# Kernel optimization log

Hardware: AMD Instinct MI355X
Metric: run time of the kernel (lower is better)

The kernel has to match this reference:

```python
import jax, jax.numpy as jnp
import numpy as np
from jax import lax

N = 8192

def _conv(x, w, b):
    # x: NCHW, w: OIHW, valid conv stride 1
    y = lax.conv_general_dilated(x, w, (1, 1), 'VALID',
                                 dimension_numbers=('NCHW', 'OIHW', 'NCHW'))
    return y + b[None, :, None, None]

def _maxpool2(x):
    return lax.reduce_window(x, -jnp.inf, lax.max, (1, 1, 2, 2), (1, 1, 2, 2), 'VALID')

def setup_inputs() -> dict:
    key = jax.random.key(0)
    ks = jax.random.split(key, 13)
    def rn(k, shape, scale):
        return jax.random.normal(k, shape, dtype=jnp.float32) * scale
    inp = {}
    inp['x'] = jax.random.normal(ks[0], (N, 3, 32, 32), dtype=jnp.float32)
    inp['W1'] = rn(ks[1], (6, 3, 5, 5), 0.1)
    inp['b1'] = rn(ks[2], (6,), 0.1)
    inp['W2'] = rn(ks[3], (16, 6, 5, 5), 0.08)
    inp['b2'] = rn(ks[4], (16,), 0.1)
    inp['Wf1'] = rn(ks[5], (120, 400), 0.05)
    inp['bf1'] = rn(ks[6], (120,), 0.05)
    inp['Wf2'] = rn(ks[7], (84, 120), 0.09)
    inp['bf2'] = rn(ks[8], (84,), 0.09)
    inp['Wg'] = rn(ks[9], (10, 84), 0.1)    # GATConv fc weight (no bias)
    inp['attn_l'] = rn(ks[10], (10,), 0.3)  # a_l (src)
    inp['attn_r'] = rn(ks[11], (10,), 0.3)  # a_r (dst)
    inp['bg'] = rn(ks[12], (10,), 0.1)      # GATConv output bias
    return inp

def reference(x, W1, b1, W2, b2, Wf1, bf1, Wf2, bf2, Wg, attn_l, attn_r, bg):
    # CNN feature extractor (LeNet style)
    h = _maxpool2(jax.nn.relu(_conv(x, W1, b1)))   # [N,6,14,14]
    h = _maxpool2(jax.nn.relu(_conv(h, W2, b2)))   # [N,16,5,5]
    h = h.reshape(-1, 16 * 5 * 5)                  # [N,400]
    h = jax.nn.relu(h @ Wf1.T + bf1)               # [N,120]
    h = jax.nn.relu(h @ Wf2.T + bf2)               # [N,84]
    # Single-head GAT over fully-connected graph (incl. self-loops):
    # equivalent dense formulation of DGL GATConv(84,10,1)
    z = h @ Wg.T                                    # [N,10]
    el = z @ attn_l                                 # src scores [N]
    er = z @ attn_r                                 # dst scores [N]
    # e[i,j]: edge src=j -> dst=i
    e = jax.nn.leaky_relu(er[:, None] + el[None, :], negative_slope=0.2)  # [N,N]
    alpha = jax.nn.softmax(e, axis=1)               # softmax over incoming edges
    out = alpha @ z + bg                            # [N,10]
    return out
```

## Files before the change

### kernel.cpp

```cpp
#include <hip/hip_runtime.h>
#include <hip/hip_bf16.h>

typedef _Float16 half8 __attribute__((ext_vector_type(8)));
typedef __attribute__((aligned(8))) half8 half8_a8;
typedef float floatx4 __attribute__((ext_vector_type(4)));

#define LOG2E 1.44269504088896340736f

__device__ __forceinline__ float pool4_dpp(float v) {
  int s1 = __builtin_amdgcn_update_dpp(0, __float_as_int(v), 0xB1, 0xF, 0xF, true);
  float v1 = fmaxf(v, __int_as_float(s1));
  int s2 = __builtin_amdgcn_update_dpp(0, __float_as_int(v1), 0x4E, 0xF, 0xF, true);
  return fmaxf(v1, __int_as_float(s2));
}

__device__ __forceinline__ unsigned f2mono(float f) {
  unsigned u = __float_as_uint(f);
  return (u & 0x80000000u) ? ~u : (u | 0x80000000u);
}
__device__ __forceinline__ float mono2f(unsigned u) {
  return (u & 0x80000000u) ? __uint_as_float(u & 0x7fffffffu)
                           : __uint_as_float(~u);
}

__global__ __launch_bounds__(256) void k_prep(const float* __restrict__ Wf1,
    const float* __restrict__ Wf2, const float* __restrict__ Wg,
    const float* __restrict__ W1, const float* __restrict__ W2,
    _Float16* __restrict__ w1f, _Float16* __restrict__ w2f,
    _Float16* __restrict__ wgf, _Float16* __restrict__ B1,
    _Float16* __restrict__ B2M, unsigned* __restrict__ emx) {
  const int i = blockIdx.x * 256 + threadIdx.x;
  if (i == 0) emx[0] = 0u;
  if (i < 53248) {
    const int n = i / 416, k = i - n * 416;
    w1f[i] = (_Float16)((n < 120 && k < 400) ? Wf1[n * 400 + k] : 0.f);
  } else if (i < 65536) {
    const int j = i - 53248;
    const int n = j >> 7, k = j & 127;
    w2f[j] = (_Float16)((n < 84 && k < 120) ? Wf2[n * 120 + k] : 0.f);
  } else if (i < 67072) {
    const int g = i - 65536;
    const int n = g / 96, k = g - n * 96;
    wgf[g] = (_Float16)((n < 10 && k < 84) ? Wg[n * 84 + k] : 0.f);
  } else if (i < 73216) {
    const int g = i - 67072;
    const int n = g / 192, k = g - n * 192;
    const int co = n >> 2, cy = (n >> 1) & 1, cx = n & 1;
    const int pidx = k >> 3, j = k & 7;
    const int r = pidx >> 2, ci = pidx & 3;
    float v = 0.f;
    if (co < 6 && ci < 3) {
      const int ky = r - cy, kx = j - cx;
      if (ky >= 0 && ky < 5 && kx >= 0 && kx < 5)
        v = W1[((co * 3 + ci) * 5 + ky) * 5 + kx];
    }
    B1[g] = (_Float16)v;
  } else if (i < 77312) {
    const int g = i - 73216;
    const int n = g >> 8, k = g & 255;
    float v = 0.f;
    if (k < 240) {
      const int ci = k / 40, rem = k - ci * 40, r = rem >> 3, j = rem & 7;
      if (j < 5) v = W2[((n * 6 + ci) * 5 + r) * 5 + j];
    }
    B2M[g] = (_Float16)v;
  }
}

__global__ __launch_bounds__(512) void k_convs(const float* __restrict__ x,
    const _Float16* __restrict__ B1, const float* __restrict__ b1,
    const _Float16* __restrict__ B2M, const float* __restrict__ b2,
    _Float16* __restrict__ h2) {
  __shared__ __align__(16) char sm[71616];
  _Float16* h1L = (_Float16*)(sm + 62208);
  const int t = threadIdx.x;
  const int n0 = blockIdx.x * 4;
  const int w8 = t >> 6, lane = t & 63;
  const int l16 = lane & 15, q = lane >> 4;

  const float4* x4 = (const float4*)(x + (size_t)n0 * 3072);
  for (int i = t; i < 3072; i += 512) {
    const float4 v = x4[i];
    const int img = i / 768;
    const int ii = i - img * 768;
    const int ci = ii >> 8, rem2 = ii & 255;
    const int y = rem2 >> 3, c = rem2 & 7;
    union { _Float16 h[2]; unsigned u; } p01, p23;
    p01.h[0] = (_Float16)v.x; p01.h[1] = (_Float16)v.y;
    p23.h[0] = (_Float16)v.z; p23.h[1] = (_Float16)v.w;
    char* row = sm + img * 15552 + ci * 5184 + y * 80;
    *(uint2*)(row + 8 * c) = make_uint2(p01.u, p23.u);
    *(unsigned*)(row + 2596 + 8 * c) = p01.u;
    *(unsigned*)(row + 2600 + 8 * c) = p23.u;
  }
  if (t < 384) {
    const int img = t / 96, tt = t - img * 96;
    const int ci = tt >> 5, y = tt & 31;
    *(unsigned*)(sm + img * 15552 + ci * 5184 + 2596 + y * 80 + 64) = 0u;
  }
  if (t < 64) {
    const int im = t >> 4;
    h2[(size_t)(n0 + im) * 416 + 400 + (t & 15)] = (_Float16)0.f;
  }
  __syncthreads();

  {
    const int img = w8 >> 1, wl = w8 & 1;
    const int px = l16;
    const int colOff = (px & 1) ? (2596 + 4 * px) : (4 * px);
    const char* base = sm + img * 15552 + ((q == 3) ? 0 : q * 5184) + colOff;
    half8 bfr[2][6];
#pragma unroll
    for (int nt = 0; nt < 2; nt++)
#pragma unroll
      for (int kc = 0; kc < 6; kc++)
        bfr[nt][kc] =
            *(const half8*)(B1 + (size_t)(nt * 16 + l16) * 192 + kc * 32 + q * 8);
    const int co_n = l16 >> 2;
    const int co1 = 4 + co_n;
    const float bias0 = b1[co_n];
    const float bias1 = (co1 < 6) ? b1[co1] : 0.f;
    const int py0 = wl * 7;
    const int py1 = py0 + 7;
    half8 a[6];
#pragma unroll
    for (int r = 0; r < 6; r++)
      a[r] = *(const half8_a8*)(base + (2 * py0 + r) * 80);
    _Float16* dstb = h1L + img * 1176;
    const bool store_lane = (l16 & 3) == 0;
    for (int py = py0; py < py1; ++py) {
      floatx4 acc0, acc1;
#pragma unroll
      for (int r = 0; r < 4; r++) { acc0[r] = 0.f; acc1[r] = 0.f; }
#pragma unroll
      for (int kc = 0; kc < 6; kc++) {
        acc0 = __builtin_amdgcn_mfma_f32_16x16x32_f16(a[kc], bfr[0][kc], acc0, 0, 0, 0);
        acc1 = __builtin_amdgcn_mfma_f32_16x16x32_f16(a[kc], bfr[1][kc], acc1, 0, 0, 0);
      }
      if (py < py1 - 1) {
        a[0] = a[2]; a[1] = a[3]; a[2] = a[4]; a[3] = a[5];
        a[4] = *(const half8_a8*)(base + (2 * py + 6) * 80);
        a[5] = *(const half8_a8*)(base + (2 * py + 7) * 80);
      }
      float p0[4], p1[4];
#pragma unroll
      for (int r = 0; r < 4; r++) {
        p0[r] = fmaxf(pool4_dpp(acc0[r]) + bias0, 0.f);
        p1[r] = fmaxf(pool4_dpp(acc1[r]) + bias1, 0.f);
      }
      if (store_lane) {
        union { _Float16 h[2]; unsigned u; } s01, s23;
        s01.h[0] = (_Float16)p0[0]; s01.h[1] = (_Float16)p0[1];
        s23.h[0] = (_Float16)p0[2]; s23.h[1] = (_Float16)p0[3];
        _Float16* dst = dstb + co_n * 196 + py * 14 + q * 4;
        *(unsigned*)dst = s01.u;
        if (q < 3) *(unsigned*)(dst + 2) = s23.u;
        if (co1 < 6) {
          union { _Float16 h[2]; unsigned u; } t01, t23;
          t01.h[0] = (_Float16)p1[0]; t01.h[1] = (_Float16)p1[1];
          t23.h[0] = (_Float16)p1[2]; t23.h[1] = (_Float16)p1[3];
          _Float16* dst1 = dstb + co1 * 196 + py * 14 + q * 4;
          *(unsigned*)dst1 = t01.u;
          if (q < 3) *(unsigned*)(dst1 + 2) = t23.u;
        }
      }
    }
  }
  __syncthreads();

  if (t < 336) {
    const int img = t / 84, rem = t - img * 84;
    const int ci = rem / 14, y = rem - ci * 14;
    const unsigned* src = (const unsigned*)(h1L + img * 1176 + ci * 196 + y * 14);
    unsigned u[10];
#pragma unroll
    for (int k = 0; k < 7; k++) u[k] = src[k];
    u[7] = 0u; u[8] = 0u; u[9] = 0u;
    char* base = sm + img * 11184 + ci * 1864 + y * 32;
#pragma unroll
    for (int ww = 0; ww < 8; ww++) {
      *(unsigned*)(base + 4 * ww) = u[ww];
      *(unsigned*)(base + 464 + 4 * ww) = (u[ww] >> 16) | (u[ww + 1] << 16);
      *(unsigned*)(base + 928 + 4 * ww) = u[ww + 1];
      *(unsigned*)(base + 1392 + 4 * ww) = (u[ww + 1] >> 16) | (u[ww + 2] << 16);
    }
  }
  __syncthreads();

  {
    int C2[8];
#pragma unroll
    for (int kc = 0; kc < 8; kc++) {
      const int pidx = kc * 4 + q;
      C2[kc] = (pidx < 30) ? (pidx / 5) * 1864 + (pidx % 5) * 32 : 0;
    }
    half8 bfr[8];
#pragma unroll
    for (int kc = 0; kc < 8; kc++)
      bfr[kc] = *(const half8*)(B2M + (size_t)l16 * 256 + kc * 32 + q * 8);
    const float bias = b2[l16];
    for (int mt = w8; mt < 26; mt += 8) {
      const int m = min(mt * 16 + l16, 399);
      const int pos = m >> 2, cy = (m >> 1) & 1, cx = m & 1;
      const int img = pos / 25, p = pos - img * 25;
      const int py = p / 5, px = p - py * 5;
      const int h = 2 * px + cx, s = h & 3;
      const char* base =
          sm + img * 11184 + s * 464 + (2 * py + cy) * 32 + (h - s) * 2;
      half8 a[8];
#pragma unroll
      for (int kc = 0; kc < 8; kc++) a[kc] = *(const half8_a8*)(base + C2[kc]);
      floatx4 acc;
#pragma unroll
      for (int r = 0; r < 4; r++) acc[r] = 0.f;
#pragma unroll
      for (int kc = 0; kc < 8; kc++)
        acc = __builtin_amdgcn_mfma_f32_16x16x32_f16(a[kc], bfr[kc], acc, 0, 0, 0);
      const float v = fmaxf(fmaxf(acc[0], acc[1]), fmaxf(acc[2], acc[3]));
      const int posL = mt * 4 + q;
      if (posL < 100) {
        const int im = posL / 25, pp = posL - im * 25;
        h2[(size_t)(n0 + im) * 416 + l16 * 25 + pp] =
            (_Float16)fmaxf(v + bias, 0.f);
      }
    }
  }
}

__global__ __launch_bounds__(256) void k_mlp(
    const _Float16* __restrict__ h2, const _Float16* __restrict__ w1,
    const float* __restrict__ bf1, const _Float16* __restrict__ w2,
    const float* __restrict__ bf2, const _Float16* __restrict__ wg,
    const float* __restrict__ al, const float* __restrict__ ar,
    _Float16* __restrict__ zT, float* __restrict__ el, float* __restrict__ er,
    unsigned* __restrict__ emx) {
  __shared__ __align__(16) _Float16 h3s[32 * 136];
  __shared__ __align__(16) _Float16 h4s[32 * 104];
  __shared__ float zs[32 * 17];
  const int t = threadIdx.x;
  const int w = t >> 6, lane = t & 63;
  const int l16 = lane & 15, q = lane >> 4;
  const int row0 = blockIdx.x * 32;
  for (int i = t; i < 2176; i += 256) ((float*)h3s)[i] = 0.f;
  for (int i = t; i < 1664; i += 256) ((float*)h4s)[i] = 0.f;
  const int rt = w & 1, cg = w >> 1;
  const int am = row0 + rt * 16 + l16;
  floatx4 acc[4];
#pragma unroll
  for (int ct = 0; ct < 4; ct++)
#pragma unroll
    for (int r = 0; r < 4; r++) acc[ct][r] = 0.f;
  const half8* Ag = (const half8*)(h2 + (size_t)am * 416 + q * 8);
  for (int kc = 0; kc < 13; kc++) {
    half8 a = Ag[kc * 4];
#pragma unroll
    for (int ct = 0; ct < 4; ct++) {
      const int n = cg * 64 + ct * 16 + l16;
      half8 b = *(const half8*)(w1 + (size_t)n * 416 + kc * 32 + q * 8);
      acc[ct] = __builtin_amdgcn_mfma_f32_16x16x32_f16(a, b, acc[ct], 0, 0, 0);
    }
  }
  __syncthreads();
#pragma unroll
  for (int ct = 0; ct < 4; ct++) {
    const int n = cg * 64 + ct * 16 + l16;
    if (n < 120) {
      const float bias = bf1[n];
#pragma unroll
      for (int r = 0; r < 4; r++) {
        const int rr = rt * 16 + q * 4 + r;
        h3s[rr * 136 + n] = (_Float16)fmaxf(acc[ct][r] + bias, 0.f);
      }
    }
  }
  __syncthreads();
  const int cbase2 = (w >> 1) * 3;
  floatx4 acc2[3];
#pragma unroll
  for (int ct = 0; ct < 3; ct++)
#pragma unroll
    for (int r = 0; r < 4; r++) acc2[ct][r] = 0.f;
  const _Float16* A2 = h3s + (rt * 16 + l16) * 136 + q * 8;
  for (int kc = 0; kc < 4; kc++) {
    half8 a = *(const half8*)(A2 + kc * 32);
#pragma unroll
    for (int ct = 0; ct < 3; ct++) {
      const int n = (cbase2 + ct) * 16 + l16;
      half8 b = *(const half8*)(w2 + (size_t)n * 128 + kc * 32 + q * 8);
      acc2[ct] = __builtin_amdgcn_mfma_f32_16x16x32_f16(a, b, acc2[ct], 0, 0, 0);
    }
  }
  __syncthreads();
#pragma unroll
  for (int ct = 0; ct < 3; ct++) {
    const int n = (cbase2 + ct) * 16 + l16;
    if (n < 84) {
      const float bias = bf2[n];
#pragma unroll
      for (int r = 0; r < 4; r++) {
        const int rr = rt * 16 + q * 4 + r;
        h4s[rr * 104 + n] = (_Float16)fmaxf(acc2[ct][r] + bias, 0.f);
      }
    }
  }
  __syncthreads();
  if (w < 2) {
    floatx4 acc3;
#pragma unroll
    for (int r = 0; r < 4; r++) acc3[r] = 0.f;
    const _Float16* A3 = h4s + (w * 16 + l16) * 104 + q * 8;
    for (int kc = 0; kc < 3; kc++) {
      half8 a = *(const half8*)(A3 + kc * 32);
      half8 b = *(const half8*)(wg + (size_t)l16 * 96 + kc * 32 + q * 8);
      acc3 = __builtin_amdgcn_mfma_f32_16x16x32_f16(a, b, acc3, 0, 0, 0);
    }
#pragma unroll
    for (int r = 0; r < 4; r++) {
      const int rr = w * 16 + q * 4 + r;
      zs[rr * 17 + l16] = acc3[r];
    }
  }
  __syncthreads();
  if (t < 32) {
    float e1 = 0.f, e2 = 0.f;
#pragma unroll
    for (int d = 0; d < 10; d++) {
      const float zv = zs[t * 17 + d];
      e1 += zv * al[d];
      e2 += zv * ar[d];
    }
    const float elv = e1 * LOG2E;
    el[row0 + t] = elv;
    er[row0 + t] = e2 * LOG2E;
    float m = elv;
#pragma unroll
    for (int off = 16; off > 0; off >>= 1)
      m = fmaxf(m, __shfl_down(m, off, 32));
    if (t == 0) atomicMax(emx, f2mono(m));
  }
  for (int idx = t; idx < 352; idx += 256) {
    const int d = idx >> 5, c = idx & 31;
    zT[(size_t)d * 8192 + row0 + c] =
        (d < 10) ? (_Float16)zs[c * 17 + d] : (_Float16)1.0f;
  }
}

__global__ __launch_bounds__(1024) void k_attn(const _Float16* __restrict__ zT,
    const float* __restrict__ el, const float* __restrict__ er,
    const unsigned* __restrict__ emx, const float* __restrict__ bg,
    float* __restrict__ out) {
  __shared__ float red[8][2][16][12];
  const int t = threadIdx.x;
  const int w = t >> 6, lane = t & 63;
  const int l16 = lane & 15, q = lane >> 4;
  const int isub = w & 1, js = w >> 1;
  const int row0 = blockIdx.x * 32;
  const int itile = row0 + isub * 16;
  const int jb = js * 1024;
  const float mx = mono2f(emx[0]);
  const float eri = er[itile + l16];
  const float s0 = eri + mx;
  const float mi = fmaxf(s0, 0.2f * s0);
  floatx4 acc;
#pragma unroll
  for (int r = 0; r < 4; r++) acc[r] = 0.f;
  const float* elp = el + jb + q * 8;
  const _Float16* ztp = zT + (size_t)l16 * 8192 + jb + q * 8;
  for (int jc = 0; jc < 32; jc++) {
    const float4 e0 = *(const float4*)(elp + jc * 32);
    const float4 e1 = *(const float4*)(elp + jc * 32 + 4);
    float wf[8];
    const float ej[8] = {e0.x, e0.y, e0.z, e0.w, e1.x, e1.y, e1.z, e1.w};
#pragma unroll
    for (int u = 0; u < 8; u++) {
      const float s = eri + ej[u];
      const float lr = fmaxf(s, 0.2f * s);
      wf[u] = exp2f(lr - mi);
    }
    half8 a;
#pragma unroll
    for (int u = 0; u < 8; u++) a[u] = (_Float16)wf[u];
    const half8 b = *(const half8*)(ztp + jc * 32);
    acc = __builtin_amdgcn_mfma_f32_16x16x32_f16(a, b, acc, 0, 0, 0);
  }
  if (l16 < 11) {
#pragma unroll
    for (int r = 0; r < 4; r++) red[js][isub][q * 4 + r][l16] = acc[r];
  }
  __syncthreads();
  if (t < 320) {
    const int ii = t / 10, d = t - (t / 10) * 10;
    const int i1 = ii >> 4, i2 = ii & 15;
    float num = 0.f, den = 0.f;
#pragma unroll
    for (int s = 0; s < 8; s++) {
      num += red[s][i1][i2][d];
      den += red[s][i1][i2][10];
    }
    out[(size_t)(row0 + ii) * 10 + d] = num / den + bg[d];
  }
}

extern "C" void kernel_launch(void* const* d_in, const int* in_sizes, int n_in,
                              void* d_out, int out_size, void* d_ws, size_t ws_size,
                              hipStream_t stream) {
  const float* x   = (const float*)d_in[0];
  const float* W1  = (const float*)d_in[1];
  const float* b1  = (const float*)d_in[2];
  const float* W2  = (const float*)d_in[3];
  const float* b2  = (const float*)d_in[4];
  const float* Wf1 = (const float*)d_in[5];
  const float* bf1 = (const float*)d_in[6];
  const float* Wf2 = (const float*)d_in[7];
  const float* bf2 = (const float*)d_in[8];
  const float* Wg  = (const float*)d_in[9];
  const float* al  = (const float*)d_in[10];
  const float* ar  = (const float*)d_in[11];
  const float* bg  = (const float*)d_in[12];
  float* out = (float*)d_out;

  float* ws = (float*)d_ws;
  float* p = ws + (size_t)8192 * 588;
  _Float16* h2f = (_Float16*)p;
  p += (size_t)8192 * 208;
  _Float16* zTf = (_Float16*)p; p += 65536;
  float* el  = p; p += 8192;
  float* er  = p; p += 8192;
  unsigned* emx = (unsigned*)p; p += 16;
  _Float16* w1f = (_Float16*)p; p += 26624;
  _Float16* w2f = (_Float16*)p; p += 6144;
  _Float16* wgf = (_Float16*)p; p += 768;
  _Float16* B1g = (_Float16*)p; p += 3072;
  _Float16* B2g = (_Float16*)p; p += 2048;

  k_prep<<<302, 256, 0, stream>>>(Wf1, Wf2, Wg, W1, W2, w1f, w2f, wgf, B1g, B2g, emx);
  k_convs<<<2048, 512, 0, stream>>>(x, B1g, b1, B2g, b2, h2f);
  k_mlp<<<256, 256, 0, stream>>>(h2f, w1f, bf1, w2f, bf2, wgf, al, ar, zTf, el, er, emx);
  k_attn<<<256, 1024, 0, stream>>>(zTf, el, er, emx, bg, out);
}
```

Baseline: 256.6 us.

## Process one image per conv block with smaller LDS footprint and padded strides

The fused conv kernel now handles one image per 256-thread block instead of four images per 512-thread block, which shrinks shared memory from about 72KB to about 18KB. The aim is to fit more blocks per CU and raise occupancy. The LDS strides for the input planes and the shifted conv2 staging buffers are also re-padded (5200, 560/2240, 40-byte rows), probably to cut bank conflicts. In exchange, work splits unevenly across the 4 waves: 14 conv1 rows become 3/4/3/4, and 7 conv2 M-tiles cover only 25 positions, leaving some lanes idle. Per-block setup cost is also amortized over fewer images.

Measured after the change: 274.0 us. 1.07x slower.

```diff
diff --git a/kernel.cpp b/kernel.cpp
--- a/kernel.cpp
+++ b/kernel.cpp
@@ -67,48 +67,43 @@
   }
 }
 
-__global__ __launch_bounds__(512) void k_convs(const float* __restrict__ x,
+__global__ __launch_bounds__(256) void k_convs(const float* __restrict__ x,
     const _Float16* __restrict__ B1, const float* __restrict__ b1,
     const _Float16* __restrict__ B2M, const float* __restrict__ b2,
     _Float16* __restrict__ h2) {
-  __shared__ __align__(16) char sm[71616];
-  _Float16* h1L = (_Float16*)(sm + 62208);
+  __shared__ __align__(16) char sm[17952];
+  _Float16* h1L = (_Float16*)(sm + 15600);
   const int t = threadIdx.x;
-  const int n0 = blockIdx.x * 4;
-  const int w8 = t >> 6, lane = t & 63;
+  const int n0 = blockIdx.x;
+  const int w4 = t >> 6, lane = t & 63;
   const int l16 = lane & 15, q = lane >> 4;
 
   const float4* x4 = (const float4*)(x + (size_t)n0 * 3072);
-  for (int i = t; i < 3072; i += 512) {
+  for (int i = t; i < 768; i += 256) {
     const float4 v = x4[i];
-    const int img = i / 768;
-    const int ii = i - img * 768;
-    const int ci = ii >> 8, rem2 = ii & 255;
+    const int ci = i >> 8, rem2 = i & 255;
     const int y = rem2 >> 3, c = rem2 & 7;
     union { _Float16 h[2]; unsigned u; } p01, p23;
     p01.h[0] = (_Float16)v.x; p01.h[1] = (_Float16)v.y;
     p23.h[0] = (_Float16)v.z; p23.h[1] = (_Float16)v.w;
-    char* row = sm + img * 15552 + ci * 5184 + y * 80;
+    char* row = sm + ci * 5200 + y * 80;
     *(uint2*)(row + 8 * c) = make_uint2(p01.u, p23.u);
     *(unsigned*)(row + 2596 + 8 * c) = p01.u;
     *(unsigned*)(row + 2600 + 8 * c) = p23.u;
   }
-  if (t < 384) {
-    const int img = t / 96, tt = t - img * 96;
-    const int ci = tt >> 5, y = tt & 31;
-    *(unsigned*)(sm + img * 15552 + ci * 5184 + 2596 + y * 80 + 64) = 0u;
-  }
-  if (t < 64) {
-    const int im = t >> 4;
-    h2[(size_t)(n0 + im) * 416 + 400 + (t & 15)] = (_Float16)0.f;
+  if (t < 96) {
+    const int ci = t >> 5, y = t & 31;
+    *(unsigned*)(sm + ci * 5200 + 2596 + y * 80 + 64) = 0u;
+  }
+  if (t < 16) {
+    h2[(size_t)n0 * 416 + 400 + t] = (_Float16)0.f;
   }
   __syncthreads();
 
   {
-    const int img = w8 >> 1, wl = w8 & 1;
     const int px = l16;
     const int colOff = (px & 1) ? (2596 + 4 * px) : (4 * px);
-    const char* base = sm + img * 15552 + ((q == 3) ? 0 : q * 5184) + colOff;
+    const char* base = sm + ((q == 3) ? 0 : q * 5200) + colOff;
     half8 bfr[2][6];
 #pragma unroll
     for (int nt = 0; nt < 2; nt++)
@@ -120,13 +115,12 @@
     const int co1 = 4 + co_n;
     const float bias0 = b1[co_n];
     const float bias1 = (co1 < 6) ? b1[co1] : 0.f;
-    const int py0 = wl * 7;
-    const int py1 = py0 + 7;
+    const int py0 = (7 * w4) >> 1;
+    const int py1 = (7 * (w4 + 1)) >> 1;
     half8 a[6];
 #pragma unroll
     for (int r = 0; r < 6; r++)
       a[r] = *(const half8_a8*)(base + (2 * py0 + r) * 80);
-    _Float16* dstb = h1L + img * 1176;
     const bool store_lane = (l16 & 3) == 0;
     for (int py = py0; py < py1; ++py) {
       floatx4 acc0, acc1;
@@ -152,14 +146,14 @@
         union { _Float16 h[2]; unsigned u; } s01, s23;
         s01.h[0] = (_Float16)p0[0]; s01.h[1] = (_Float16)p0[1];
         s23.h[0] = (_Float16)p0[2]; s23.h[1] = (_Float16)p0[3];
-        _Float16* dst = dstb + co_n * 196 + py * 14 + q * 4;
+        _Float16* dst = h1L + co_n * 196 + py * 14 + q * 4;
         *(unsigned*)dst = s01.u;
         if (q < 3) *(unsigned*)(dst + 2) = s23.u;
         if (co1 < 6) {
           union { _Float16 h[2]; unsigned u; } t01, t23;
           t01.h[0] = (_Float16)p1[0]; t01.h[1] = (_Float16)p1[1];
           t23.h[0] = (_Float16)p1[2]; t23.h[1] = (_Float16)p1[3];
-          _Float16* dst1 = dstb + co1 * 196 + py * 14 + q * 4;
+          _Float16* dst1 = h1L + co1 * 196 + py * 14 + q * 4;
           *(unsigned*)dst1 = t01.u;
           if (q < 3) *(unsigned*)(dst1 + 2) = t23.u;
         }
@@ -168,21 +162,23 @@
   }
   __syncthreads();
 
-  if (t < 336) {
-    const int img = t / 84, rem = t - img * 84;
-    const int ci = rem / 14, y = rem - ci * 14;
-    const unsigned* src = (const unsigned*)(h1L + img * 1176 + ci * 196 + y * 14);
-    unsigned u[10];
-#pragma unroll
-    for (int k = 0; k < 7; k++) u[k] = src[k];
-    u[7] = 0u; u[8] = 0u; u[9] = 0u;
-    char* base = sm + img * 11184 + ci * 1864 + y * 32;
-#pragma unroll
-    for (int ww = 0; ww < 8; ww++) {
+  if (t < 168) {
+    const int ci = t / 28, rem = t - ci * 28;
+    const int y = rem >> 1, g = rem & 1;
+    const unsigned* src = (const unsigned*)(h1L + ci * 196 + y * 14);
+    unsigned u[6];
+#pragma unroll
+    for (int k = 0; k < 6; k++) {
+      const int idx = 4 * g + k;
+      u[k] = (idx < 7) ? src[idx] : 0u;
+    }
+    char* base = sm + ci * 2240 + y * 40 + 16 * g;
+#pragma unroll
+    for (int ww = 0; ww < 4; ww++) {
       *(unsigned*)(base + 4 * ww) = u[ww];
-      *(unsigned*)(base + 464 + 4 * ww) = (u[ww] >> 16) | (u[ww + 1] << 16);
-      *(unsigned*)(base + 928 + 4 * ww) = u[ww + 1];
-      *(unsigned*)(base + 1392 + 4 * ww) = (u[ww + 1] >> 16) | (u[ww + 2] << 16);
+      *(unsigned*)(base + 560 + 4 * ww) = (u[ww] >> 16) | (u[ww + 1] << 16);
+      *(unsigned*)(base + 1120 + 4 * ww) = u[ww + 1];
+      *(unsigned*)(base + 1680 + 4 * ww) = (u[ww + 1] >> 16) | (u[ww + 2] << 16);
     }
   }
   __syncthreads();
@@ -192,21 +188,19 @@
 #pragma unroll
     for (int kc = 0; kc < 8; kc++) {
       const int pidx = kc * 4 + q;
-      C2[kc] = (pidx < 30) ? (pidx / 5) * 1864 + (pidx % 5) * 32 : 0;
+      C2[kc] = (pidx < 30) ? (pidx / 5) * 2240 + (pidx % 5) * 40 : 0;
     }
     half8 bfr[8];
 #pragma unroll
     for (int kc = 0; kc < 8; kc++)
       bfr[kc] = *(const half8*)(B2M + (size_t)l16 * 256 + kc * 32 + q * 8);
     const float bias = b2[l16];
-    for (int mt = w8; mt < 26; mt += 8) {
-      const int m = min(mt * 16 + l16, 399);
+    for (int mt = w4; mt < 7; mt += 4) {
+      const int m = min(mt * 16 + l16, 99);
       const int pos = m >> 2, cy = (m >> 1) & 1, cx = m & 1;
-      const int img = pos / 25, p = pos - img * 25;
-      const int py = p / 5, px = p - py * 5;
+      const int py = pos / 5, px = pos - py * 5;
       const int h = 2 * px + cx, s = h & 3;
-      const char* base =
-          sm + img * 11184 + s * 464 + (2 * py + cy) * 32 + (h - s) * 2;
+      const char* base = sm + s * 560 + (2 * py + cy) * 40 + (h - s) * 2;
       half8 a[8];
 #pragma unroll
       for (int kc = 0; kc < 8; kc++) a[kc] = *(const half8_a8*)(base + C2[kc]);
@@ -218,9 +212,8 @@
         acc = __builtin_amdgcn_mfma_f32_16x16x32_f16(a[kc], bfr[kc], acc, 0, 0, 0);
       const float v = fmaxf(fmaxf(acc[0], acc[1]), fmaxf(acc[2], acc[3]));
       const int posL = mt * 4 + q;
-      if (posL < 100) {
-        const int im = posL / 25, pp = posL - im * 25;
-        h2[(size_t)(n0 + im) * 416 + l16 * 25 + pp] =
+      if (posL < 25) {
+        h2[(size_t)n0 * 416 + l16 * 25 + posL] =
             (_Float16)fmaxf(v + bias, 0.f);
       }
     }
@@ -434,7 +427,7 @@
   _Float16* B2g = (_Float16*)p; p += 2048;
 
   k_prep<<<302, 256, 0, stream>>>(Wf1, Wf2, Wg, W1, W2, w1f, w2f, wgf, B1g, B2g, emx);
-  k_convs<<<2048, 512, 0, stream>>>(x, B1g, b1, B2g, b2, h2f);
+  k_convs<<<8192, 256, 0, stream>>>(x, B1g, b1, B2g, b2, h2f);
   k_mlp<<<256, 256, 0, stream>>>(h2f, w1f, bf1, w2f, bf2, wgf, al, ar, zTf, el, er, emx);
   k_attn<<<256, 1024, 0, stream>>>(zTf, el, er, emx, bg, out);
 }
```

## Shrink conv blocks to three images and 256 threads for higher occupancy

Applied to the files above, without the earlier changes.

The fused conv kernel now processes three images per block with 256 threads, cutting LDS from about 70KB to about 53KB so three blocks can share a CU (launch_bounds 256,3). Work is redistributed: conv1 rows are assigned per wave across images with full reloads of the six A rows instead of a sliding window, the re-layout step is split into half-row tasks, and weight fragments are hoisted to kernel start. Bounds checks handle the partial last block. This trades some redundant LDS reads and register pressure for better latency hiding from more resident waves.

Result: no change. 261.7 us (+2.0%).

```diff
diff --git a/kernel.cpp b/kernel.cpp
--- a/kernel.cpp
+++ b/kernel.cpp
@@ -67,21 +67,39 @@
   }
 }
 
-__global__ __launch_bounds__(512) void k_convs(const float* __restrict__ x,
+__global__ __launch_bounds__(256, 3) void k_convs(const float* __restrict__ x,
     const _Float16* __restrict__ B1, const float* __restrict__ b1,
     const _Float16* __restrict__ B2M, const float* __restrict__ b2,
     _Float16* __restrict__ h2) {
-  __shared__ __align__(16) char sm[71616];
-  _Float16* h1L = (_Float16*)(sm + 62208);
+  __shared__ __align__(16) char sm[53712];
+  _Float16* h1L = (_Float16*)(sm + 46656);
   const int t = threadIdx.x;
-  const int n0 = blockIdx.x * 4;
-  const int w8 = t >> 6, lane = t & 63;
+  const int n0 = blockIdx.x * 3;
+  const int w4 = t >> 6, lane = t & 63;
   const int l16 = lane & 15, q = lane >> 4;
 
+  half8 bfr1[2][6];
+#pragma unroll
+  for (int nt = 0; nt < 2; nt++)
+#pragma unroll
+    for (int kc = 0; kc < 6; kc++)
+      bfr1[nt][kc] =
+          *(const half8*)(B1 + (size_t)(nt * 16 + l16) * 192 + kc * 32 + q * 8);
+  half8 bfr2[8];
+#pragma unroll
+  for (int kc = 0; kc < 8; kc++)
+    bfr2[kc] = *(const half8*)(B2M + (size_t)l16 * 256 + kc * 32 + q * 8);
+  const int co_n = l16 >> 2;
+  const int co1 = 4 + co_n;
+  const float bias1_0 = b1[co_n];
+  const float bias1_1 = (co1 < 6) ? b1[co1] : 0.f;
+  const float bias2 = b2[l16];
+
   const float4* x4 = (const float4*)(x + (size_t)n0 * 3072);
-  for (int i = t; i < 3072; i += 512) {
-    const float4 v = x4[i];
+  for (int i = t; i < 2304; i += 256) {
     const int img = i / 768;
+    float4 v = make_float4(0.f, 0.f, 0.f, 0.f);
+    if (n0 + img < 8192) v = x4[i];
     const int ii = i - img * 768;
     const int ci = ii >> 8, rem2 = ii & 255;
     const int y = rem2 >> 3, c = rem2 & 7;
@@ -93,73 +111,60 @@
     *(unsigned*)(row + 2596 + 8 * c) = p01.u;
     *(unsigned*)(row + 2600 + 8 * c) = p23.u;
   }
-  if (t < 384) {
+  if (t < 192) {
     const int img = t / 96, tt = t - img * 96;
     const int ci = tt >> 5, y = tt & 31;
     *(unsigned*)(sm + img * 15552 + ci * 5184 + 2596 + y * 80 + 64) = 0u;
-  }
-  if (t < 64) {
+    if (t < 96) {
+      const int ci2 = t >> 5, y2 = t & 31;
+      *(unsigned*)(sm + 2 * 15552 + ci2 * 5184 + 2596 + y2 * 80 + 64) = 0u;
+    }
+  }
+  if (t < 48) {
     const int im = t >> 4;
-    h2[(size_t)(n0 + im) * 416 + 400 + (t & 15)] = (_Float16)0.f;
+    if (n0 + im < 8192)
+      h2[(size_t)(n0 + im) * 416 + 400 + (t & 15)] = (_Float16)0.f;
   }
   __syncthreads();
 
   {
-    const int img = w8 >> 1, wl = w8 & 1;
     const int px = l16;
     const int colOff = (px & 1) ? (2596 + 4 * px) : (4 * px);
-    const char* base = sm + img * 15552 + ((q == 3) ? 0 : q * 5184) + colOff;
-    half8 bfr[2][6];
-#pragma unroll
-    for (int nt = 0; nt < 2; nt++)
-#pragma unroll
-      for (int kc = 0; kc < 6; kc++)
-        bfr[nt][kc] =
-            *(const half8*)(B1 + (size_t)(nt * 16 + l16) * 192 + kc * 32 + q * 8);
-    const int co_n = l16 >> 2;
-    const int co1 = 4 + co_n;
-    const float bias0 = b1[co_n];
-    const float bias1 = (co1 < 6) ? b1[co1] : 0.f;
-    const int py0 = wl * 7;
-    const int py1 = py0 + 7;
-    half8 a[6];
-#pragma unroll
-    for (int r = 0; r < 6; r++)
-      a[r] = *(const half8_a8*)(base + (2 * py0 + r) * 80);
-    _Float16* dstb = h1L + img * 1176;
+    const char* cbase = sm + ((q == 3) ? 0 : q * 5184) + colOff;
     const bool store_lane = (l16 & 3) == 0;
-    for (int py = py0; py < py1; ++py) {
+    for (int u = w4; u < 42; u += 4) {
+      const int img = u / 14, py = u - img * 14;
+      const char* base = cbase + img * 15552;
+      half8 a[6];
+#pragma unroll
+      for (int r = 0; r < 6; r++)
+        a[r] = *(const half8_a8*)(base + (2 * py + r) * 80);
       floatx4 acc0, acc1;
 #pragma unroll
       for (int r = 0; r < 4; r++) { acc0[r] = 0.f; acc1[r] = 0.f; }
 #pragma unroll
       for (int kc = 0; kc < 6; kc++) {
-        acc0 = __builtin_amdgcn_mfma_f32_16x16x32_f16(a[kc], bfr[0][kc], acc0, 0, 0, 0);
-        acc1 = __builtin_amdgcn_mfma_f32_16x16x32_f16(a[kc], bfr[1][kc], acc1, 0, 0, 0);
-      }
-      if (py < py1 - 1) {
-        a[0] = a[2]; a[1] = a[3]; a[2] = a[4]; a[3] = a[5];
-        a[4] = *(const half8_a8*)(base + (2 * py + 6) * 80);
-        a[5] = *(const half8_a8*)(base + (2 * py + 7) * 80);
+        acc0 = __builtin_amdgcn_mfma_f32_16x16x32_f16(a[kc], bfr1[0][kc], acc0, 0, 0, 0);
+        acc1 = __builtin_amdgcn_mfma_f32_16x16x32_f16(a[kc], bfr1[1][kc], acc1, 0, 0, 0);
       }
       float p0[4], p1[4];
 #pragma unroll
       for (int r = 0; r < 4; r++) {
-        p0[r] = fmaxf(pool4_dpp(acc0[r]) + bias0, 0.f);
-        p1[r] = fmaxf(pool4_dpp(acc1[r]) + bias1, 0.f);
+        p0[r] = fmaxf(pool4_dpp(acc0[r]) + bias1_0, 0.f);
+        p1[r] = fmaxf(pool4_dpp(acc1[r]) + bias1_1, 0.f);
       }
       if (store_lane) {
         union { _Float16 h[2]; unsigned u; } s01, s23;
         s01.h[0] = (_Float16)p0[0]; s01.h[1] = (_Float16)p0[1];
         s23.h[0] = (_Float16)p0[2]; s23.h[1] = (_Float16)p0[3];
-        _Float16* dst = dstb + co_n * 196 + py * 14 + q * 4;
+        _Float16* dst = h1L + img * 1176 + co_n * 196 + py * 14 + q * 4;
         *(unsigned*)dst = s01.u;
         if (q < 3) *(unsigned*)(dst + 2) = s23.u;
         if (co1 < 6) {
           union { _Float16 h[2]; unsigned u; } t01, t23;
           t01.h[0] = (_Float16)p1[0]; t01.h[1] = (_Float16)p1[1];
           t23.h[0] = (_Float16)p1[2]; t23.h[1] = (_Float16)p1[3];
-          _Float16* dst1 = dstb + co1 * 196 + py * 14 + q * 4;
+          _Float16* dst1 = h1L + img * 1176 + co1 * 196 + py * 14 + q * 4;
           *(unsigned*)dst1 = t01.u;
           if (q < 3) *(unsigned*)(dst1 + 2) = t23.u;
         }
@@ -168,21 +173,24 @@
   }
   __syncthreads();
 
-  if (t < 336) {
-    const int img = t / 84, rem = t - img * 84;
-    const int ci = rem / 14, y = rem - ci * 14;
+  for (int uu = t; uu < 504; uu += 256) {
+    const int img = uu / 168, rem = uu - img * 168;
+    const int ci = rem / 28, r2 = rem - ci * 28;
+    const int y = r2 >> 1, g = r2 & 1;
     const unsigned* src = (const unsigned*)(h1L + img * 1176 + ci * 196 + y * 14);
-    unsigned u[10];
-#pragma unroll
-    for (int k = 0; k < 7; k++) u[k] = src[k];
-    u[7] = 0u; u[8] = 0u; u[9] = 0u;
-    char* base = sm + img * 11184 + ci * 1864 + y * 32;
-#pragma unroll
-    for (int ww = 0; ww < 8; ww++) {
-      *(unsigned*)(base + 4 * ww) = u[ww];
-      *(unsigned*)(base + 464 + 4 * ww) = (u[ww] >> 16) | (u[ww + 1] << 16);
-      *(unsigned*)(base + 928 + 4 * ww) = u[ww + 1];
-      *(unsigned*)(base + 1392 + 4 * ww) = (u[ww + 1] >> 16) | (u[ww + 2] << 16);
+    unsigned u6[6];
+#pragma unroll
+    for (int k = 0; k < 6; k++) {
+      const int idx = 4 * g + k;
+      u6[k] = (idx < 7) ? src[idx] : 0u;
+    }
+    char* base = sm + img * 11136 + ci * 1856 + y * 32 + 16 * g;
+#pragma unroll
+    for (int ww = 0; ww < 4; ww++) {
+      *(unsigned*)(base + 4 * ww) = u6[ww];
+      *(unsigned*)(base + 464 + 4 * ww) = (u6[ww] >> 16) | (u6[ww + 1] << 16);
+      *(unsigned*)(base + 928 + 4 * ww) = u6[ww + 1];
+      *(unsigned*)(base + 1392 + 4 * ww) = (u6[ww + 1] >> 16) | (u6[ww + 2] << 16);
     }
   }
   __syncthreads();
@@ -192,21 +200,16 @@
 #pragma unroll
     for (int kc = 0; kc < 8; kc++) {
       const int pidx = kc * 4 + q;
-      C2[kc] = (pidx < 30) ? (pidx / 5) * 1864 + (pidx % 5) * 32 : 0;
-    }
-    half8 bfr[8];
-#pragma unroll
-    for (int kc = 0; kc < 8; kc++)
-      bfr[kc] = *(const half8*)(B2M + (size_t)l16 * 256 + kc * 32 + q * 8);
-    const float bias = b2[l16];
-    for (int mt = w8; mt < 26; mt += 8) {
-      const int m = min(mt * 16 + l16, 399);
+      C2[kc] = (pidx < 30) ? (pidx / 5) * 1856 + (pidx % 5) * 32 : 0;
+    }
+    for (int mt = w4; mt < 19; mt += 4) {
+      const int m = min(mt * 16 + l16, 299);
       const int pos = m >> 2, cy = (m >> 1) & 1, cx = m & 1;
       const int img = pos / 25, p = pos - img * 25;
       const int py = p / 5, px = p - py * 5;
       const int h = 2 * px + cx, s = h & 3;
       const char* base =
-          sm + img * 11184 + s * 464 + (2 * py + cy) * 32 + (h - s) * 2;
+          sm + img * 11136 + s * 464 + (2 * py + cy) * 32 + (h - s) * 2;
       half8 a[8];
 #pragma unroll
       for (int kc = 0; kc < 8; kc++) a[kc] = *(const half8_a8*)(base + C2[kc]);
@@ -215,13 +218,14 @@
       for (int r = 0; r < 4; r++) acc[r] = 0.f;
 #pragma unroll
       for (int kc = 0; kc < 8; kc++)
-        acc = __builtin_amdgcn_mfma_f32_16x16x32_f16(a[kc], bfr[kc], acc, 0, 0, 0);
+        acc = __builtin_amdgcn_mfma_f32_16x16x32_f16(a[kc], bfr2[kc], acc, 0, 0, 0);
       const float v = fmaxf(fmaxf(acc[0], acc[1]), fmaxf(acc[2], acc[3]));
       const int posL = mt * 4 + q;
-      if (posL < 100) {
+      if (posL < 75) {
         const int im = posL / 25, pp = posL - im * 25;
-        h2[(size_t)(n0 + im) * 416 + l16 * 25 + pp] =
-            (_Float16)fmaxf(v + bias, 0.f);
+        if (n0 + im < 8192)
+          h2[(size_t)(n0 + im) * 416 + l16 * 25 + pp] =
+              (_Float16)fmaxf(v + bias2, 0.f);
       }
     }
   }
@@ -434,7 +438,7 @@
   _Float16* B2g = (_Float16*)p; p += 2048;
 
   k_prep<<<302, 256, 0, stream>>>(Wf1, Wf2, Wg, W1, W2, w1f, w2f, wgf, B1g, B2g, emx);
-  k_convs<<<2048, 512, 0, stream>>>(x, B1g, b1, B2g, b2, h2f);
+  k_convs<<<2731, 256, 0, stream>>>(x, B1g, b1, B2g, b2, h2f);
   k_mlp<<<256, 256, 0, stream>>>(h2f, w1f, bf1, w2f, bf2, wgf, al, ar, zTf, el, er, emx);
   k_attn<<<256, 1024, 0, stream>>>(zTf, el, er, emx, bg, out);
 }
```

## Halve conv block to two images and restripe conv2 shared layout

Applied to the files above, without the earlier changes.

The fused conv kernel now handles 2 images per 256-thread block instead of 4 per 512 threads. That halves shared memory per block, so more blocks can be resident per CU, with a launch-bounds hint of 4 blocks. The conv2 im2col staging is rewritten: rows are padded to 40 bytes, work is split across two half-rows per thread, and stores are wider 8-byte writes. Conv1 output stores are also merged into 8-byte writes. The trade-off is twice as many blocks and more redundant weight fragment loads per image.

After: 252.4 us. No clear change (-1.6%).

```diff
diff --git a/kernel.cpp b/kernel.cpp
--- a/kernel.cpp
+++ b/kernel.cpp
@@ -67,21 +67,21 @@
   }
 }
 
-__global__ __launch_bounds__(512) void k_convs(const float* __restrict__ x,
+__global__ __launch_bounds__(256, 4) void k_convs(const float* __restrict__ x,
     const _Float16* __restrict__ B1, const float* __restrict__ b1,
     const _Float16* __restrict__ B2M, const float* __restrict__ b2,
     _Float16* __restrict__ h2) {
-  __shared__ __align__(16) char sm[71616];
-  _Float16* h1L = (_Float16*)(sm + 62208);
+  __shared__ __align__(16) char sm[35808];
+  _Float16* h1L = (_Float16*)(sm + 31104);
   const int t = threadIdx.x;
-  const int n0 = blockIdx.x * 4;
-  const int w8 = t >> 6, lane = t & 63;
+  const int n0 = blockIdx.x * 2;
+  const int w4 = t >> 6, lane = t & 63;
   const int l16 = lane & 15, q = lane >> 4;
 
   const float4* x4 = (const float4*)(x + (size_t)n0 * 3072);
-  for (int i = t; i < 3072; i += 512) {
+  for (int i = t; i < 1536; i += 256) {
     const float4 v = x4[i];
-    const int img = i / 768;
+    const int img = (i >= 768);
     const int ii = i - img * 768;
     const int ci = ii >> 8, rem2 = ii & 255;
     const int y = rem2 >> 3, c = rem2 & 7;
@@ -93,19 +93,19 @@
     *(unsigned*)(row + 2596 + 8 * c) = p01.u;
     *(unsigned*)(row + 2600 + 8 * c) = p23.u;
   }
-  if (t < 384) {
+  if (t < 192) {
     const int img = t / 96, tt = t - img * 96;
     const int ci = tt >> 5, y = tt & 31;
     *(unsigned*)(sm + img * 15552 + ci * 5184 + 2596 + y * 80 + 64) = 0u;
   }
-  if (t < 64) {
+  if (t < 32) {
     const int im = t >> 4;
     h2[(size_t)(n0 + im) * 416 + 400 + (t & 15)] = (_Float16)0.f;
   }
   __syncthreads();
 
   {
-    const int img = w8 >> 1, wl = w8 & 1;
+    const int img = w4 >> 1, wl = w4 & 1;
     const int px = l16;
     const int colOff = (px & 1) ? (2596 + 4 * px) : (4 * px);
     const char* base = sm + img * 15552 + ((q == 3) ? 0 : q * 5184) + colOff;
@@ -153,75 +153,81 @@
         s01.h[0] = (_Float16)p0[0]; s01.h[1] = (_Float16)p0[1];
         s23.h[0] = (_Float16)p0[2]; s23.h[1] = (_Float16)p0[3];
         _Float16* dst = dstb + co_n * 196 + py * 14 + q * 4;
-        *(unsigned*)dst = s01.u;
-        if (q < 3) *(unsigned*)(dst + 2) = s23.u;
+        if (q < 3) *(uint2*)dst = make_uint2(s01.u, s23.u);
+        else *(unsigned*)dst = s01.u;
         if (co1 < 6) {
           union { _Float16 h[2]; unsigned u; } t01, t23;
           t01.h[0] = (_Float16)p1[0]; t01.h[1] = (_Float16)p1[1];
           t23.h[0] = (_Float16)p1[2]; t23.h[1] = (_Float16)p1[3];
           _Float16* dst1 = dstb + co1 * 196 + py * 14 + q * 4;
-          *(unsigned*)dst1 = t01.u;
-          if (q < 3) *(unsigned*)(dst1 + 2) = t23.u;
+          if (q < 3) *(uint2*)dst1 = make_uint2(t01.u, t23.u);
+          else *(unsigned*)dst1 = t01.u;
         }
       }
     }
   }
   __syncthreads();
 
-  if (t < 336) {
-    const int img = t / 84, rem = t - img * 84;
-    const int ci = rem / 14, y = rem - ci * 14;
+  for (int uu = t; uu < 336; uu += 256) {
+    const int img = uu / 168, rem = uu - img * 168;
+    const int ci = rem / 28, r2 = rem - ci * 28;
+    const int y = r2 >> 1, g = r2 & 1;
     const unsigned* src = (const unsigned*)(h1L + img * 1176 + ci * 196 + y * 14);
-    unsigned u[10];
-#pragma unroll
-    for (int k = 0; k < 7; k++) u[k] = src[k];
-    u[7] = 0u; u[8] = 0u; u[9] = 0u;
-    char* base = sm + img * 11184 + ci * 1864 + y * 32;
-#pragma unroll
-    for (int ww = 0; ww < 8; ww++) {
-      *(unsigned*)(base + 4 * ww) = u[ww];
-      *(unsigned*)(base + 464 + 4 * ww) = (u[ww] >> 16) | (u[ww + 1] << 16);
-      *(unsigned*)(base + 928 + 4 * ww) = u[ww + 1];
-      *(unsigned*)(base + 1392 + 4 * ww) = (u[ww + 1] >> 16) | (u[ww + 2] << 16);
-    }
+    unsigned u6[6];
+#pragma unroll
+    for (int k = 0; k < 6; k++) {
+      const int idx = 4 * g + k;
+      u6[k] = (idx < 7) ? src[idx] : 0u;
+    }
+    unsigned sh[5];
+#pragma unroll
+    for (int k = 0; k < 5; k++) sh[k] = (u6[k] >> 16) | (u6[k + 1] << 16);
+    char* bs = sm + img * 13440 + ci * 2240 + y * 40 + 16 * g;
+    *(uint2*)(bs) = make_uint2(u6[0], u6[1]);
+    *(uint2*)(bs + 8) = make_uint2(u6[2], u6[3]);
+    *(uint2*)(bs + 560) = make_uint2(sh[0], sh[1]);
+    *(uint2*)(bs + 568) = make_uint2(sh[2], sh[3]);
+    *(uint2*)(bs + 1120) = make_uint2(u6[1], u6[2]);
+    *(uint2*)(bs + 1128) = make_uint2(u6[3], u6[4]);
+    *(uint2*)(bs + 1680) = make_uint2(sh[1], sh[2]);
+    *(uint2*)(bs + 1688) = make_uint2(sh[3], sh[4]);
   }
   __syncthreads();
 
   {
+    half8 bfr2[8];
+#pragma unroll
+    for (int kc = 0; kc < 8; kc++)
+      bfr2[kc] = *(const half8*)(B2M + (size_t)l16 * 256 + kc * 32 + q * 8);
     int C2[8];
 #pragma unroll
     for (int kc = 0; kc < 8; kc++) {
       const int pidx = kc * 4 + q;
-      C2[kc] = (pidx < 30) ? (pidx / 5) * 1864 + (pidx % 5) * 32 : 0;
-    }
-    half8 bfr[8];
-#pragma unroll
-    for (int kc = 0; kc < 8; kc++)
-      bfr[kc] = *(const half8*)(B2M + (size_t)l16 * 256 + kc * 32 + q * 8);
-    const float bias = b2[l16];
-    for (int mt = w8; mt < 26; mt += 8) {
-      const int m = min(mt * 16 + l16, 399);
+      C2[kc] = (pidx < 30) ? (pidx / 5) * 2240 + (pidx % 5) * 40 : 0;
+    }
+    const float bias2 = b2[l16];
+    for (int mt = w4; mt < 13; mt += 4) {
+      const int m = min(mt * 16 + l16, 199);
       const int pos = m >> 2, cy = (m >> 1) & 1, cx = m & 1;
       const int img = pos / 25, p = pos - img * 25;
       const int py = p / 5, px = p - py * 5;
       const int h = 2 * px + cx, s = h & 3;
       const char* base =
-          sm + img * 11184 + s * 464 + (2 * py + cy) * 32 + (h - s) * 2;
-      half8 a[8];
-#pragma unroll
-      for (int kc = 0; kc < 8; kc++) a[kc] = *(const half8_a8*)(base + C2[kc]);
+          sm + img * 13440 + s * 560 + (2 * py + cy) * 40 + (h - s) * 2;
       floatx4 acc;
 #pragma unroll
       for (int r = 0; r < 4; r++) acc[r] = 0.f;
 #pragma unroll
-      for (int kc = 0; kc < 8; kc++)
-        acc = __builtin_amdgcn_mfma_f32_16x16x32_f16(a[kc], bfr[kc], acc, 0, 0, 0);
+      for (int kc = 0; kc < 8; kc++) {
+        const half8 av = *(const half8_a8*)(base + C2[kc]);
+        acc = __builtin_amdgcn_mfma_f32_16x16x32_f16(av, bfr2[kc], acc, 0, 0, 0);
+      }
       const float v = fmaxf(fmaxf(acc[0], acc[1]), fmaxf(acc[2], acc[3]));
       const int posL = mt * 4 + q;
-      if (posL < 100) {
+      if (posL < 50) {
         const int im = posL / 25, pp = posL - im * 25;
         h2[(size_t)(n0 + im) * 416 + l16 * 25 + pp] =
-            (_Float16)fmaxf(v + bias, 0.f);
+            (_Float16)fmaxf(v + bias2, 0.f);
       }
     }
   }
@@ -434,7 +440,7 @@
   _Float16* B2g = (_Float16*)p; p += 2048;
 
   k_prep<<<302, 256, 0, stream>>>(Wf1, Wf2, Wg, W1, W2, w1f, w2f, wgf, B1g, B2g, emx);
-  k_convs<<<2048, 512, 0, stream>>>(x, B1g, b1, B2g, b2, h2f);
+  k_convs<<<4096, 256, 0, stream>>>(x, B1g, b1, B2g, b2, h2f);
   k_mlp<<<256, 256, 0, stream>>>(h2f, w1f, bf1, w2f, bf2, wgf, al, ar, zTf, el, er, emx);
   k_attn<<<256, 1024, 0, stream>>>(zTf, el, er, emx, bg, out);
 }
```
